# Performance work log

Hardware: AMD Instinct MI355X
Metric: run time of the kernel (lower is better)

Reference implementation:

```python
import jax, jax.numpy as jnp
import numpy as np

B = 16384
S = 7          # grid cells per side
C = 30         # 2 boxes * 5 + 20 classes
GX = 7.0       # num_gridx = labels.shape[-2]
GY = 30.0      # num_gridy = labels.shape[-1]  (faithful to the original code's size()[-2:] bug)


def setup_inputs() -> dict:
    key = jax.random.key(0)
    k1, k2, k3 = jax.random.split(key, 3)
    # keep w,h away from 0 so sqrt grads are finite
    pred = jax.random.uniform(k1, (B, S, S, C), dtype=jnp.float32, minval=0.05, maxval=0.95)
    labels = jax.random.uniform(k2, (B, S, S, C), dtype=jnp.float32, minval=0.05, maxval=0.95)
    obj = jax.random.bernoulli(k3, 0.3, (B, S, S)).astype(jnp.float32)
    labels = labels.at[..., 4].set(obj)
    return {"pred": pred, "labels": labels}


def _boxes_xyxy(t, off, mg, ng):
    # t[..., off:off+4] = (x, y, w, h) relative to cell; convert to xyxy
    cx = (t[..., off] + mg) / GX
    cy = (t[..., off + 1] + ng) / GY
    w = t[..., off + 2]
    h = t[..., off + 3]
    return jnp.stack([cx - w / 2, cy - h / 2, cx + w / 2, cy + h / 2], axis=-1)


def _iou(b1, b2):
    ix1 = jnp.maximum(b1[..., 0], b2[..., 0])
    iy1 = jnp.maximum(b1[..., 1], b2[..., 1])
    ix2 = jnp.minimum(b1[..., 2], b2[..., 2])
    iy2 = jnp.minimum(b1[..., 3], b2[..., 3])
    iw = jnp.maximum(ix2 - ix1, 0.0)
    ih = jnp.maximum(iy2 - iy1, 0.0)
    inter = iw * ih
    a1 = (b1[..., 2] - b1[..., 0]) * (b1[..., 3] - b1[..., 1])
    a2 = (b2[..., 2] - b2[..., 0]) * (b2[..., 3] - b2[..., 1])
    union = a1 + a2 - inter
    pos = inter > 0
    return jnp.where(pos, inter / jnp.where(pos, union, 1.0), 0.0)


def reference(pred, labels):
    n_batch = pred.shape[0]
    # grid offsets: m indexes axis 1, n indexes axis 2
    mg = jnp.arange(S, dtype=pred.dtype)[:, None]   # (7,1)
    ng = jnp.arange(S, dtype=pred.dtype)[None, :]   # (1,7)

    pb1 = _boxes_xyxy(pred, 0, mg, ng)
    pb2 = _boxes_xyxy(pred, 5, mg, ng)
    gb = _boxes_xyxy(labels, 0, mg, ng)
    iou1 = _iou(pb1, gb)   # (B,7,7)
    iou2 = _iou(pb2, gb)
    sel1 = iou1 >= iou2
    obj = labels[..., 4] == 1.0

    coor1 = (jnp.sum((pred[..., 0:2] - labels[..., 0:2]) ** 2, -1)
             + jnp.sum((jnp.sqrt(pred[..., 2:4]) - jnp.sqrt(labels[..., 2:4])) ** 2, -1))
    coor2 = (jnp.sum((pred[..., 5:7] - labels[..., 5:7]) ** 2, -1)
             + jnp.sum((jnp.sqrt(pred[..., 7:9]) - jnp.sqrt(labels[..., 7:9])) ** 2, -1))
    coor = 5.0 * jnp.where(sel1, coor1, coor2)

    d1 = (pred[..., 4] - iou1) ** 2
    d2 = (pred[..., 9] - iou2) ** 2
    obj_confi = jnp.where(sel1, d1, d2)
    noobj_at_obj = 0.5 * jnp.where(sel1, d2, d1)

    class_loss = jnp.sum((pred[..., 10:] - labels[..., 10:]) ** 2, -1)

    noobj_at_noobj = 0.5 * (pred[..., 4] ** 2 + pred[..., 9] ** 2)

    per_cell = jnp.where(obj, coor + obj_confi + noobj_at_obj + class_loss, noobj_at_noobj)
    return jnp.sum(per_cell) / n_batch
```

## Files before the change

kernel.cpp:

```cpp
#include <hip/hip_runtime.h>


#define NCELLS (16384 * 49)
#define INV_NB (1.0f / 16384.0f)
#define CPB 256
#define FPA (CPB * 30)
#define F4PA (FPA / 4)

__device__ __forceinline__ float iou_xyxy(float ax1, float ay1, float ax2, float ay2,
                                          float bx1, float by1, float bx2, float by2) {
    float ix1 = fmaxf(ax1, bx1);
    float iy1 = fmaxf(ay1, by1);
    float ix2 = fminf(ax2, bx2);
    float iy2 = fminf(ay2, by2);
    float iw = fmaxf(ix2 - ix1, 0.0f);
    float ih = fmaxf(iy2 - iy1, 0.0f);
    float inter = iw * ih;
    float a1 = (ax2 - ax1) * (ay2 - ay1);
    float a2 = (bx2 - bx1) * (by2 - by1);
    float uni = a1 + a2 - inter;
    return (inter > 0.0f) ? (inter / uni) : 0.0f;
}

__global__ __launch_bounds__(256, 2) void yolo_loss_kernel(const float* __restrict__ pred,
                                                           const float* __restrict__ labels,
                                                           float* __restrict__ out) {
    __shared__ float sm[2 * FPA];

    const int t = threadIdx.x;
    const float* gp = pred + (size_t)blockIdx.x * FPA;
    const float* gl = labels + (size_t)blockIdx.x * FPA;

    float4* sm4 = reinterpret_cast<float4*>(sm);
    const float4* gp4 = reinterpret_cast<const float4*>(gp);
    const float4* gl4 = reinterpret_cast<const float4*>(gl);
#pragma unroll
    for (int i = 0; i < 15; ++i) {
        int idx = i * 256 + t;
        float4 v = (idx < F4PA) ? gp4[idx] : gl4[idx - F4PA];
        sm4[idx] = v;
    }
    __syncthreads();

    const int gcell = blockIdx.x * CPB + t;
    const int rem = gcell % 49;
    const float fm = (float)(rem / 7);
    const float fn = (float)(rem % 7);

    const float2* ps = reinterpret_cast<const float2*>(sm + t * 30);
    const float2* ls = reinterpret_cast<const float2*>(sm + FPA + t * 30);

    float pv[30], lv[30];
#pragma unroll
    for (int k = 0; k < 15; ++k) {
        float2 a = ps[k];
        pv[2 * k] = a.x; pv[2 * k + 1] = a.y;
    }
#pragma unroll
    for (int k = 0; k < 15; ++k) {
        float2 b = ls[k];
        lv[2 * k] = b.x; lv[2 * k + 1] = b.y;
    }

    float cx = (pv[0] + fm) / 7.0f;
    float cy = (pv[1] + fn) / 30.0f;
    float w = pv[2], h = pv[3];
    float p1x1 = cx - w * 0.5f, p1y1 = cy - h * 0.5f;
    float p1x2 = cx + w * 0.5f, p1y2 = cy + h * 0.5f;

    cx = (pv[5] + fm) / 7.0f;
    cy = (pv[6] + fn) / 30.0f;
    w = pv[7]; h = pv[8];
    float p2x1 = cx - w * 0.5f, p2y1 = cy - h * 0.5f;
    float p2x2 = cx + w * 0.5f, p2y2 = cy + h * 0.5f;

    cx = (lv[0] + fm) / 7.0f;
    cy = (lv[1] + fn) / 30.0f;
    w = lv[2]; h = lv[3];
    float gx1 = cx - w * 0.5f, gy1 = cy - h * 0.5f;
    float gx2 = cx + w * 0.5f, gy2 = cy + h * 0.5f;

    float iou1 = iou_xyxy(p1x1, p1y1, p1x2, p1y2, gx1, gy1, gx2, gy2);
    float iou2 = iou_xyxy(p2x1, p2y1, p2x2, p2y2, gx1, gy1, gx2, gy2);

    bool sel1 = (iou1 >= iou2);
    bool obj = (lv[4] == 1.0f);

    float dx = pv[0] - lv[0], dy = pv[1] - lv[1];
    float dw = sqrtf(pv[2]) - sqrtf(lv[2]);
    float dh = sqrtf(pv[3]) - sqrtf(lv[3]);
    float coor1 = dx * dx + dy * dy + dw * dw + dh * dh;

    dx = pv[5] - lv[5]; dy = pv[6] - lv[6];
    dw = sqrtf(pv[7]) - sqrtf(lv[7]);
    dh = sqrtf(pv[8]) - sqrtf(lv[8]);
    float coor2 = dx * dx + dy * dy + dw * dw + dh * dh;

    float coor = 5.0f * (sel1 ? coor1 : coor2);

    float d1 = pv[4] - iou1; d1 *= d1;
    float d2 = pv[9] - iou2; d2 *= d2;
    float obj_confi = sel1 ? d1 : d2;
    float noobj_at_obj = 0.5f * (sel1 ? d2 : d1);

    float cls = 0.0f;
#pragma unroll
    for (int k = 10; k < 30; ++k) {
        float d = pv[k] - lv[k];
        cls += d * d;
    }

    float noobj_at_noobj = 0.5f * (pv[4] * pv[4] + pv[9] * pv[9]);

    float per = obj ? (coor + obj_confi + noobj_at_obj + cls) : noobj_at_noobj;

    float acc = per;
#pragma unroll
    for (int off = 32; off > 0; off >>= 1) acc += __shfl_down(acc, off, 64);

    __shared__ float sbuf[4];
    int lane = t & 63;
    int wid = t >> 6;
    if (lane == 0) sbuf[wid] = acc;
    __syncthreads();
    if (t == 0) {
        float s = (sbuf[0] + sbuf[1] + sbuf[2] + sbuf[3]) * INV_NB;
        atomicAdd(out, s);
    }
}

extern "C" void kernel_launch(void* const* d_in, const int* in_sizes, int n_in,
                              void* d_out, int out_size, void* d_ws, size_t ws_size,
                              hipStream_t stream) {
    const float* pred = (const float*)d_in[0];
    const float* labels = (const float*)d_in[1];
    float* out = (float*)d_out;

    hipMemsetAsync(out, 0, sizeof(float), stream);

    const int threads = 256;
    const int blocks = NCELLS / threads;
    yolo_loss_kernel<<<blocks, threads, 0, stream>>>(pred, labels, out);
}
```

Before: 204.0 us.

## Split reduction into per-block partials plus single finalize kernel, shrink blocks to one wave

```diff
diff --git a/kernel.cpp b/kernel.cpp
--- a/kernel.cpp
+++ b/kernel.cpp
@@ -3,9 +3,10 @@
 
 #define NCELLS (16384 * 49)
 #define INV_NB (1.0f / 16384.0f)
-#define CPB 256
-#define FPA (CPB * 30)
-#define F4PA (FPA / 4)
+#define CPB 64
+#define NBLK (NCELLS / CPB)
+#define SLAB_F4 (CPB * 30 / 4)
+#define SLAB_F (CPB * 30)
 
 __device__ __forceinline__ float iou_xyxy(float ax1, float ay1, float ax2, float ay2,
                                           float bx1, float by1, float bx2, float by2) {
@@ -22,33 +23,37 @@
     return (inter > 0.0f) ? (inter / uni) : 0.0f;
 }
 
-__global__ __launch_bounds__(256, 2) void yolo_loss_kernel(const float* __restrict__ pred,
-                                                           const float* __restrict__ labels,
-                                                           float* __restrict__ out) {
-    __shared__ float sm[2 * FPA];
+__global__ __launch_bounds__(64, 2) void yolo_loss_stage1(const float* __restrict__ pred,
+                                                          const float* __restrict__ labels,
+                                                          float* __restrict__ partials) {
+    __shared__ float sm[2 * SLAB_F];
 
     const int t = threadIdx.x;
-    const float* gp = pred + (size_t)blockIdx.x * FPA;
-    const float* gl = labels + (size_t)blockIdx.x * FPA;
+    const int b = blockIdx.x;
 
-    float4* sm4 = reinterpret_cast<float4*>(sm);
-    const float4* gp4 = reinterpret_cast<const float4*>(gp);
-    const float4* gl4 = reinterpret_cast<const float4*>(gl);
+    const float4* gp4 = reinterpret_cast<const float4*>(pred) + (size_t)b * SLAB_F4;
+    const float4* gl4 = reinterpret_cast<const float4*>(labels) + (size_t)b * SLAB_F4;
+
+    float4 r[15];
 #pragma unroll
     for (int i = 0; i < 15; ++i) {
-        int idx = i * 256 + t;
-        float4 v = (idx < F4PA) ? gp4[idx] : gl4[idx - F4PA];
-        sm4[idx] = v;
+        int idx = i * 64 + t;
+        r[i] = (idx < SLAB_F4) ? gp4[idx] : gl4[idx - SLAB_F4];
+    }
+    float4* sm4 = reinterpret_cast<float4*>(sm);
+#pragma unroll
+    for (int i = 0; i < 15; ++i) {
+        sm4[i * 64 + t] = r[i];
     }
     __syncthreads();
 
-    const int gcell = blockIdx.x * CPB + t;
+    const int gcell = b * CPB + t;
     const int rem = gcell % 49;
     const float fm = (float)(rem / 7);
     const float fn = (float)(rem % 7);
 
     const float2* ps = reinterpret_cast<const float2*>(sm + t * 30);
-    const float2* ls = reinterpret_cast<const float2*>(sm + FPA + t * 30);
+    const float2* ls = reinterpret_cast<const float2*>(sm + SLAB_F + t * 30);
 
     float pv[30], lv[30];
 #pragma unroll
@@ -58,8 +63,8 @@
     }
 #pragma unroll
     for (int k = 0; k < 15; ++k) {
-        float2 b = ls[k];
-        lv[2 * k] = b.x; lv[2 * k + 1] = b.y;
+        float2 bb = ls[k];
+        lv[2 * k] = bb.x; lv[2 * k + 1] = bb.y;
     }
 
     float cx = (pv[0] + fm) / 7.0f;
@@ -117,16 +122,24 @@
     float acc = per;
 #pragma unroll
     for (int off = 32; off > 0; off >>= 1) acc += __shfl_down(acc, off, 64);
+    if (t == 0) partials[b] = acc;
+}
+
+__global__ __launch_bounds__(256) void yolo_loss_stage2(const float* __restrict__ partials,
+                                                        float* __restrict__ out) {
+    const int t = threadIdx.x;
+    float acc = 0.0f;
+#pragma unroll
+    for (int i = 0; i < NBLK / 256; ++i) {
+        acc += partials[i * 256 + t];
+    }
+#pragma unroll
+    for (int off = 32; off > 0; off >>= 1) acc += __shfl_down(acc, off, 64);
 
     __shared__ float sbuf[4];
-    int lane = t & 63;
-    int wid = t >> 6;
-    if (lane == 0) sbuf[wid] = acc;
+    if ((t & 63) == 0) sbuf[t >> 6] = acc;
     __syncthreads();
-    if (t == 0) {
-        float s = (sbuf[0] + sbuf[1] + sbuf[2] + sbuf[3]) * INV_NB;
-        atomicAdd(out, s);
-    }
+    if (t == 0) out[0] = (sbuf[0] + sbuf[1] + sbuf[2] + sbuf[3]) * INV_NB;
 }
 
 extern "C" void kernel_launch(void* const* d_in, const int* in_sizes, int n_in,
@@ -135,10 +148,8 @@
     const float* pred = (const float*)d_in[0];
     const float* labels = (const float*)d_in[1];
     float* out = (float*)d_out;
+    float* partials = (float*)d_ws;
 
-    hipMemsetAsync(out, 0, sizeof(float), stream);
-
-    const int threads = 256;
-    const int blocks = NCELLS / threads;
-    yolo_loss_kernel<<<blocks, threads, 0, stream>>>(pred, labels, out);
+    yolo_loss_stage1<<<NBLK, 64, 0, stream>>>(pred, labels, partials);
+    yolo_loss_stage2<<<1, 256, 0, stream>>>(partials, out);
 }
```

Result: no change. 203.2 us (-0.4%).
